# Kernel tuning notes

Measured on AMD Instinct MI355X. Metric: run time of the kernel, lower is better.

Reference implementation:

```python
import jax, jax.numpy as jnp
import numpy as np

ROUTES = 1152
CAPS = 10
IN_CH = 8
OUT_CH = 16
BATCH = 256
NUM_ITER = 3


def setup_inputs() -> dict:
    key = jax.random.key(0)
    kx, kw = jax.random.split(key)
    x = jax.random.normal(kx, (BATCH, ROUTES, IN_CH), dtype=jnp.float32)
    # W corresponds to nn.Parameter of shape [1, routes, caps, out, in]; leading 1 dropped.
    W = jax.random.normal(kw, (ROUTES, CAPS, OUT_CH, IN_CH), dtype=jnp.float32)
    return {"x": x, "W": W}


def _squash(s):
    # Faithful to source: sum of squares over the trailing singleton dim -> elementwise.
    sq = s * s
    return sq * s / ((1.0 + sq) * jnp.sqrt(sq))


def reference(x, W):
    # u_hat[b,r,c,o] = W[r,c,o,i] @ x[b,r,i]
    u_hat = jnp.einsum("rcoi,bri->brco", W, x)
    b_ij = jnp.zeros((ROUTES, CAPS), dtype=x.dtype)
    v = None
    for it in range(NUM_ITER):
        # legacy F.softmax on 4D [1,R,C,1] tensor -> softmax over dim=1 (routes)
        c_ij = jax.nn.softmax(b_ij, axis=0)  # [R, C]
        s_j = jnp.einsum("rc,brco->bco", c_ij, u_hat)  # [B, C, O]
        v = _squash(s_j)
        if it < NUM_ITER - 1:
            # a_ij[b,r,c] = <u_hat[b,r,c,:], v[b,c,:]>; b_ij += mean over batch
            a_ij = jnp.einsum("brco,bco->brc", u_hat, v)
            b_ij = b_ij + a_ij.mean(axis=0)
    # original returns v_j.squeeze(1) with shape [B, caps, out, 1]
    return v[..., None]
```

## Files before the change

### kernel.cpp

```cpp
#include <hip/hip_runtime.h>
#include <math.h>

namespace {

constexpr int B_ = 256;
constexpr int R_ = 1152;
constexpr int C_ = 10;
constexpr int O_ = 16;
constexpr int I_ = 8;
constexpr int CO_ = C_ * O_;
constexpr int WRI_ = C_ * O_ * I_;

constexpr int KS_  = 64;
constexpr int RC_  = R_ / KS_;

constexpr int NRP_ = 576;
constexpr int NBA_ = NRP_ * 2;

constexpr int KSF_ = 16;
constexpr int RCF_ = R_ / KSF_;
constexpr int MBF_ = 16;

constexpr size_t XT_OFF    = 0;
constexpr size_t XT_N      = (size_t)R_ * B_ * I_;
constexpr size_t SA_OFF    = XT_OFF + XT_N;
constexpr size_t SAB_N     = (size_t)CO_ * B_;
constexpr size_t SB_OFF    = SA_OFF + SAB_N;
constexpr size_t BIJ_OFF   = SB_OFF + SAB_N;
constexpr size_t BIJ_N     = (size_t)C_ * R_;
constexpr size_t ZERO_N    = 2 * SAB_N + BIJ_N;
constexpr size_t FL_TOTAL  = BIJ_OFF + BIJ_N;

__device__ __forceinline__ float rcp_fast(float x) {
#if defined(__has_builtin)
#if __has_builtin(__builtin_amdgcn_rcpf)
    return __builtin_amdgcn_rcpf(x);
#else
    return 1.0f / x;
#endif
#else
    return 1.0f / x;
#endif
}

__device__ __forceinline__ float squashf(float s) {
    return s * fabsf(s) / (1.0f + s * s);
}

__device__ __forceinline__ float squash_fast(float s) {
    return s * fabsf(s) * rcp_fast(1.0f + s * s);
}

__global__ __launch_bounds__(256) void k_tr(const float* __restrict__ x,
                                            float* __restrict__ xT,
                                            float* __restrict__ zbase) {
    __shared__ float t[8][32][8];
    const int tid = threadIdx.x;
    {
        const int gi = blockIdx.x * 256 + tid;
        if (gi < (int)(ZERO_N / 4))
            ((float4*)zbase)[gi] = make_float4(0.f, 0.f, 0.f, 0.f);
    }
    const int r0 = (blockIdx.x % 36) * 32;
    const int b0 = (blockIdx.x / 36) * 8;
    {
        const int rl = tid & 31, bl = tid >> 5;
        const float4* p = (const float4*)(x + ((size_t)(b0 + bl) * R_ + (r0 + rl)) * I_);
        const float4 a0 = p[0], a1 = p[1];
        float* d = &t[bl][rl][0];
        *(float4*)d = a0;
        *(float4*)(d + 4) = a1;
    }
    __syncthreads();
    {
        const int f = tid & 7, rw = tid >> 3;
        const float* s8 = &t[f][rw][0];
        const float4 a0 = *(const float4*)s8, a1 = *(const float4*)(s8 + 4);
        float* d = xT + ((size_t)(r0 + rw) * B_ + (b0 + f)) * I_;
        *(float4*)d = a0;
        *(float4*)(d + 4) = a1;
    }
}

template <bool UNIFORM>
__global__ __launch_bounds__(256) void k_s8(const float* __restrict__ xT,
                                            const float* __restrict__ Wm,
                                            const float* __restrict__ bijT,
                                            float* __restrict__ s_dst) {
    __shared__ __align__(16) float wl[RC_ * 128];
    __shared__ float cwch[RC_];
    __shared__ float sred[8];

    const int tid   = threadIdx.x;
    const int lane  = tid & 63;
    const int bid   = blockIdx.x;
    const int c     = bid >> 7;
    const int chunk = bid & 127;
    const int ks    = chunk >> 1;
    const int bh    = chunk & 1;
    const int r0    = ks * RC_;

    if (!UNIFORM) {
        const float* bc = bijT + (size_t)c * R_;
        float bv[5];
        float m = -1e30f;
        #pragma unroll
        for (int k = 0; k < 5; ++k) {
            const int r = tid + 256 * k;
            bv[k] = (r < R_) ? bc[r] : -1e30f;
            m = fmaxf(m, bv[k]);
        }
        #pragma unroll
        for (int off = 32; off > 0; off >>= 1)
            m = fmaxf(m, __shfl_down(m, off, 64));
        if (lane == 0) sred[tid >> 6] = m;
        __syncthreads();
        const float bm = fmaxf(fmaxf(sred[0], sred[1]), fmaxf(sred[2], sred[3]));
        float se = 0.f;
        #pragma unroll
        for (int k = 0; k < 5; ++k)
            se += (bv[k] > -1e29f) ? expf(bv[k] - bm) : 0.f;
        #pragma unroll
        for (int off = 32; off > 0; off >>= 1)
            se += __shfl_down(se, off, 64);
        if (lane == 0) sred[4 + (tid >> 6)] = se;
        __syncthreads();
        const float inv = 1.0f / (sred[4] + sred[5] + sred[6] + sred[7]);
        if (tid < RC_) cwch[tid] = expf(bc[r0 + tid] - bm) * inv;
        __syncthreads();
    }

    {
        const float4* src = (const float4*)(Wm + ((size_t)r0 * C_ + c) * 128);
        float4* dst = (float4*)wl;
        #pragma unroll
        for (int k = 0; k < (RC_ * 32 + 255) / 256; ++k) {
            const int idx = tid + 256 * k;
            if (idx < RC_ * 32) {
                const int r = idx >> 5, q = idx & 31;
                float4 wv = src[(size_t)r * (C_ * 32) + q];
                const float cw = UNIFORM ? (1.0f / (float)R_) : cwch[r];
                wv.x *= cw; wv.y *= cw; wv.z *= cw; wv.w *= cw;
                dst[idx] = wv;
            }
        }
    }
    __syncthreads();

    const int o0 = (tid >> 6) * 4;
    const float* xbase = xT + ((size_t)r0 * B_ + bh * 128 + lane) * I_;

    float acc[4][2];
    #pragma unroll
    for (int oo = 0; oo < 4; ++oo) { acc[oo][0] = 0.f; acc[oo][1] = 0.f; }

    #pragma unroll 2
    for (int r = 0; r < RC_; ++r) {
        const float* xr = xbase + (size_t)r * B_ * I_;
        const float4 a00 = ((const float4*)xr)[0];
        const float4 a01 = ((const float4*)xr)[1];
        const float4 a10 = ((const float4*)(xr + 64 * I_))[0];
        const float4 a11 = ((const float4*)(xr + 64 * I_))[1];
        const float4* wp = (const float4*)&wl[r * 128 + o0 * 8];
        #pragma unroll
        for (int oo = 0; oo < 4; ++oo) {
            const float4 w0 = wp[oo * 2 + 0];
            const float4 w1 = wp[oo * 2 + 1];
            float a = acc[oo][0];
            a = fmaf(a00.x, w0.x, a);
            a = fmaf(a00.y, w0.y, a);
            a = fmaf(a00.z, w0.z, a);
            a = fmaf(a00.w, w0.w, a);
            a = fmaf(a01.x, w1.x, a);
            a = fmaf(a01.y, w1.y, a);
            a = fmaf(a01.z, w1.z, a);
            a = fmaf(a01.w, w1.w, a);
            acc[oo][0] = a;
            float b = acc[oo][1];
            b = fmaf(a10.x, w0.x, b);
            b = fmaf(a10.y, w0.y, b);
            b = fmaf(a10.z, w0.z, b);
            b = fmaf(a10.w, w0.w, b);
            b = fmaf(a11.x, w1.x, b);
            b = fmaf(a11.y, w1.y, b);
            b = fmaf(a11.z, w1.z, b);
            b = fmaf(a11.w, w1.w, b);
            acc[oo][1] = b;
        }
    }

    float* sp = s_dst + (size_t)(c * O_ + o0) * B_ + bh * 128 + lane;
    #pragma unroll
    for (int oo = 0; oo < 4; ++oo) {
        atomicAdd(sp + (size_t)oo * B_, acc[oo][0]);
        atomicAdd(sp + (size_t)oo * B_ + 64, acc[oo][1]);
    }
}

struct A9Sh {
    float4 xsw[2 * 256];
    float  part[2][320];
};

__global__ __launch_bounds__(320) void k_a9(const float* __restrict__ xT,
                                            const float* __restrict__ Wm,
                                            const float* __restrict__ s_read,
                                            float* __restrict__ s_zero,
                                            float* __restrict__ bijT) {
    __shared__ A9Sh sh;
    const int tid = threadIdx.x;
    const int bid = blockIdx.x;
    const int bh  = (bid >= NRP_) ? 1 : 0;
    const int rp  = bid - bh * NRP_;
    const int r0  = rp * 2;

    if (s_zero != nullptr && bid < 40 && tid < 256) {
        ((float4*)s_zero)[bid * 256 + tid] = make_float4(0.f, 0.f, 0.f, 0.f);
    }

    {
        const float4* src = (const float4*)(xT + (size_t)r0 * B_ * I_);
        for (int k = tid; k < 2 * 256; k += 320) {
            const int rr = k >> 8, rem = k & 255;
            sh.xsw[k ^ ((k >> 5) & 7)] = src[rr * 512 + bh * 256 + rem];
        }
    }
    __syncthreads();

    const int cq = tid % 40;
    const int bg = tid / 40;
    const int b0 = bg * 16;

    float acc[2][4][8];
    #pragma unroll
    for (int rr = 0; rr < 2; ++rr)
        #pragma unroll
        for (int j = 0; j < 4; ++j)
            #pragma unroll
            for (int i = 0; i < 8; ++i) acc[rr][j][i] = 0.f;

    const float* vbase = s_read + (size_t)(4 * cq) * B_ + bh * 128 + b0;

    #pragma unroll 2
    for (int bb = 0; bb < 16; bb += 4) {
        float va[4][4];
        #pragma unroll
        for (int j = 0; j < 4; ++j) {
            const float4 t = *(const float4*)(vbase + (size_t)j * B_ + bb);
            va[j][0] = squash_fast(t.x);
            va[j][1] = squash_fast(t.y);
            va[j][2] = squash_fast(t.z);
            va[j][3] = squash_fast(t.w);
        }
        #pragma unroll
        for (int j2 = 0; j2 < 4; ++j2) {
            const int eb = (b0 + bb + j2) * 2;
            #pragma unroll
            for (int rr = 0; rr < 2; ++rr) {
                const float4 x0 = sh.xsw[(rr * 256 + eb) ^ bg];
                const float4 x1 = sh.xsw[(rr * 256 + eb + 1) ^ bg];
                #pragma unroll
                for (int j = 0; j < 4; ++j) {
                    const float w = va[j][j2];
                    acc[rr][j][0] = fmaf(w, x0.x, acc[rr][j][0]);
                    acc[rr][j][1] = fmaf(w, x0.y, acc[rr][j][1]);
                    acc[rr][j][2] = fmaf(w, x0.z, acc[rr][j][2]);
                    acc[rr][j][3] = fmaf(w, x0.w, acc[rr][j][3]);
                    acc[rr][j][4] = fmaf(w, x1.x, acc[rr][j][4]);
                    acc[rr][j][5] = fmaf(w, x1.y, acc[rr][j][5]);
                    acc[rr][j][6] = fmaf(w, x1.z, acc[rr][j][6]);
                    acc[rr][j][7] = fmaf(w, x1.w, acc[rr][j][7]);
                }
            }
        }
    }

    #pragma unroll
    for (int rr = 0; rr < 2; ++rr) {
        const float* wp = Wm + (((size_t)(r0 + rr)) * CO_ + 4 * cq) * I_;
        float psum = 0.f;
        #pragma unroll
        for (int j = 0; j < 4; ++j) {
            const float4 w0 = *(const float4*)(wp + j * 8);
            const float4 w1 = *(const float4*)(wp + j * 8 + 4);
            float p = acc[rr][j][0] * w0.x;
            p = fmaf(acc[rr][j][1], w0.y, p);
            p = fmaf(acc[rr][j][2], w0.z, p);
            p = fmaf(acc[rr][j][3], w0.w, p);
            p = fmaf(acc[rr][j][4], w1.x, p);
            p = fmaf(acc[rr][j][5], w1.y, p);
            p = fmaf(acc[rr][j][6], w1.z, p);
            p = fmaf(acc[rr][j][7], w1.w, p);
            psum += p;
        }
        sh.part[rr][tid] = psum;
    }
    __syncthreads();

    if (tid < 2 * C_) {
        const int r = tid / C_, c2 = tid % C_;
        float s = 0.f;
        #pragma unroll
        for (int g2 = 0; g2 < 8; ++g2)
            #pragma unroll
            for (int q = 0; q < 4; ++q)
                s += sh.part[r][g2 * 40 + c2 * 4 + q];
        atomicAdd(&bijT[(size_t)c2 * R_ + (r0 + r)], s * (1.0f / (float)B_));
    }
}

__global__ __launch_bounds__(256) void k_sqout(const float* __restrict__ s,
                                               float* __restrict__ out) {
    const int co = blockIdx.x;
    const int b  = threadIdx.x;
    out[(size_t)b * CO_ + co] = squash_fast(s[(size_t)co * B_ + b]);
}

template <bool UNIFORM>
__global__ __launch_bounds__(256) void k_s_f(const float* __restrict__ x,
                                             const float* __restrict__ Wm,
                                             const float* __restrict__ cij,
                                             float* __restrict__ s_out) {
    const int o  = threadIdx.x & 15;
    const int tb = threadIdx.x >> 4;
    const int b  = blockIdx.z * MBF_ + tb;
    const int c  = blockIdx.y;
    const int r0 = blockIdx.x * RCF_;

    const float* xp = x + ((size_t)b * R_ + r0) * I_;
    const float* wp = Wm + (((size_t)r0 * C_ + c) * O_ + o) * I_;
    const float* cp = cij + (size_t)r0 * C_ + c;

    float acc = 0.f;
    #pragma unroll 4
    for (int r = 0; r < RCF_; ++r) {
        const float4 xv0 = *(const float4*)(xp);
        const float4 xv1 = *(const float4*)(xp + 4);
        const float4 wv0 = *(const float4*)(wp);
        const float4 wv1 = *(const float4*)(wp + 4);
        const float p0 = fmaf(xv0.y, wv0.y, xv0.x * wv0.x);
        const float p1 = fmaf(xv0.w, wv0.w, xv0.z * wv0.z);
        const float p2 = fmaf(xv1.y, wv1.y, xv1.x * wv1.x);
        const float p3 = fmaf(xv1.w, wv1.w, xv1.z * wv1.z);
        const float cw = UNIFORM ? (1.0f / (float)R_) : cp[0];
        acc = fmaf(cw, (p0 + p1) + (p2 + p3), acc);
        xp += I_;
        wp += WRI_;
        cp += C_;
    }
    atomicAdd(&s_out[((size_t)b * C_ + c) * O_ + o], acc);
}

__global__ __launch_bounds__(256) void k_a_f(const float* __restrict__ x,
                                             const float* __restrict__ Wm,
                                             const float* __restrict__ s_in,
                                             float* __restrict__ amean) {
    __shared__ __align__(16) float wlds[2 * WRI_];
    __shared__ float red[4][2 * C_];

    const int tid = threadIdx.x;
    const int r0  = blockIdx.x * 2;

    const float* wsrc = Wm + (size_t)r0 * WRI_;
    #pragma unroll
    for (int k = 0; k < 2 * WRI_ / 256; ++k)
        wlds[tid + 256 * k] = wsrc[tid + 256 * k];
    __syncthreads();

    const int b    = tid;
    const int lane = tid & 63;
    const int wv   = tid >> 6;

    float xv[2][I_];
    const float4* xp4 = (const float4*)(x + ((size_t)b * R_ + r0) * I_);
    #pragma unroll
    for (int rr = 0; rr < 2; ++rr) {
        const float4 a0 = xp4[rr * 2 + 0];
        const float4 a1 = xp4[rr * 2 + 1];
        xv[rr][0] = a0.x; xv[rr][1] = a0.y; xv[rr][2] = a0.z; xv[rr][3] = a0.w;
        xv[rr][4] = a1.x; xv[rr][5] = a1.y; xv[rr][6] = a1.z; xv[rr][7] = a1.w;
    }

    #pragma unroll 1
    for (int c = 0; c < C_; ++c) {
        const float4* sp4 = (const float4*)(s_in + ((size_t)b * C_ + c) * O_);
        float v[O_];
        #pragma unroll
        for (int q = 0; q < 4; ++q) {
            const float4 sv = sp4[q];
            v[q * 4 + 0] = squashf(sv.x);
            v[q * 4 + 1] = squashf(sv.y);
            v[q * 4 + 2] = squashf(sv.z);
            v[q * 4 + 3] = squashf(sv.w);
        }
        #pragma unroll 1
        for (int rr = 0; rr < 2; ++rr) {
            const float4* wl4 = (const float4*)&wlds[(rr * C_ + c) * O_ * I_];
            float a = 0.f;
            #pragma unroll
            for (int o = 0; o < O_; ++o) {
                const float4 w0 = wl4[o * 2 + 0];
                const float4 w1 = wl4[o * 2 + 1];
                float u = xv[rr][0] * w0.x;
                u = fmaf(xv[rr][1], w0.y, u);
                u = fmaf(xv[rr][2], w0.z, u);
                u = fmaf(xv[rr][3], w0.w, u);
                u = fmaf(xv[rr][4], w1.x, u);
                u = fmaf(xv[rr][5], w1.y, u);
                u = fmaf(xv[rr][6], w1.z, u);
                u = fmaf(xv[rr][7], w1.w, u);
                a = fmaf(u, v[o], a);
            }
            #pragma unroll
            for (int off = 32; off > 0; off >>= 1)
                a += __shfl_down(a, off, 64);
            if (lane == 0) red[wv][rr * C_ + c] = a;
        }
    }

    __syncthreads();
    if (tid < 2 * C_) {
        const float t = red[0][tid] + red[1][tid] + red[2][tid] + red[3][tid];
        const int rr = tid / C_;
        const int c  = tid % C_;
        amean[(size_t)(r0 + rr) * C_ + c] = t * (1.0f / (float)B_);
    }
}

__global__ __launch_bounds__(256) void k_soft(const float* __restrict__ amean,
                                              float* __restrict__ bij,
                                              float* __restrict__ cij) {
    const int c   = blockIdx.x;
    const int tid = threadIdx.x;
    __shared__ float sred[4];

    float vals[5];
    float m = -1e30f;
    #pragma unroll
    for (int k = 0; k < 5; ++k) {
        const int r = tid + 256 * k;
        if (r < R_) {
            const size_t idx = (size_t)r * C_ + c;
            const float vv = bij[idx] + amean[idx];
            bij[idx] = vv;
            vals[k] = vv;
            m = fmaxf(m, vv);
        } else {
            vals[k] = -1e30f;
        }
    }
    #pragma unroll
    for (int off = 32; off > 0; off >>= 1)
        m = fmaxf(m, __shfl_down(m, off, 64));
    if ((tid & 63) == 0) sred[tid >> 6] = m;
    __syncthreads();
    const float bm = fmaxf(fmaxf(sred[0], sred[1]), fmaxf(sred[2], sred[3]));
    __syncthreads();

    float se = 0.f;
    #pragma unroll
    for (int k = 0; k < 5; ++k)
        se += (vals[k] > -1e29f) ? expf(vals[k] - bm) : 0.f;
    #pragma unroll
    for (int off = 32; off > 0; off >>= 1)
        se += __shfl_down(se, off, 64);
    if ((tid & 63) == 0) sred[tid >> 6] = se;
    __syncthreads();
    const float inv = 1.0f / (sred[0] + sred[1] + sred[2] + sred[3]);

    #pragma unroll
    for (int k = 0; k < 5; ++k) {
        const int r = tid + 256 * k;
        if (r < R_) cij[(size_t)r * C_ + c] = expf(vals[k] - bm) * inv;
    }
}

__global__ __launch_bounds__(256) void k_squash(float* __restrict__ s) {
    const int idx = blockIdx.x * 256 + threadIdx.x;
    if (idx < B_ * CO_) s[idx] = squashf(s[idx]);
}

}

extern "C" void kernel_launch(void* const* d_in, const int* in_sizes, int n_in,
                              void* d_out, int out_size, void* d_ws, size_t ws_size,
                              hipStream_t stream) {
    const float* x  = (const float*)d_in[0];
    const float* Wm = (const float*)d_in[1];
    float* out = (float*)d_out;
    float* ws  = (float*)d_ws;

    const size_t need = FL_TOTAL * sizeof(float);

    if (ws_size >= need) {
        float* xT   = ws + XT_OFF;
        float* sA   = ws + SA_OFF;
        float* sB   = ws + SB_OFF;
        float* bijT = ws + BIJ_OFF;

        k_tr<<<1152, 256, 0, stream>>>(x, xT, sA );

        k_s8<true><<<C_ * 128, 256, 0, stream>>>(xT, Wm, bijT, sA);
        k_a9<<<NBA_, 320, 0, stream>>>(xT, Wm, sA, nullptr, bijT);

        k_s8<false><<<C_ * 128, 256, 0, stream>>>(xT, Wm, bijT, sB);
        k_a9<<<NBA_, 320, 0, stream>>>(xT, Wm, sB, sA , bijT);

        k_s8<false><<<C_ * 128, 256, 0, stream>>>(xT, Wm, bijT, sA);
        k_sqout<<<CO_, 256, 0, stream>>>(sA, out);
    } else {
        float* s_buf = ws;
        float* cij   = ws + 40960;
        float* bij   = cij + R_ * C_;
        float* amean = bij + R_ * C_;

        const dim3 gsf(KSF_, C_, B_ / MBF_);

        hipMemsetAsync(bij, 0, R_ * C_ * sizeof(float), stream);

        hipMemsetAsync(s_buf, 0, B_ * CO_ * sizeof(float), stream);
        k_s_f<true><<<gsf, 256, 0, stream>>>(x, Wm, cij, s_buf);
        k_a_f<<<R_ / 2, 256, 0, stream>>>(x, Wm, s_buf, amean);
        k_soft<<<C_, 256, 0, stream>>>(amean, bij, cij);

        hipMemsetAsync(s_buf, 0, B_ * CO_ * sizeof(float), stream);
        k_s_f<false><<<gsf, 256, 0, stream>>>(x, Wm, cij, s_buf);
        k_a_f<<<R_ / 2, 256, 0, stream>>>(x, Wm, s_buf, amean);
        k_soft<<<C_, 256, 0, stream>>>(amean, bij, cij);

        hipMemsetAsync(out, 0, B_ * CO_ * sizeof(float), stream);
        k_s_f<false><<<gsf, 256, 0, stream>>>(x, Wm, cij, out);
        k_squash<<<(B_ * CO_ + 255) / 256, 256, 0, stream>>>(out);
    }
}
```

Measured before the change: 202.0 us.

## Precompute squashed v transposed and restructure s/a kernels per route

The s-kernel now gives each block all 256 batches (4 per thread) instead of splitting the batch in halves, so each W tile is loaded and scaled once and the grid is halved. A new small transpose kernel squashes s once into a batch-major vT buffer, so the agreement kernel no longer recomputes squash per element. The agreement kernel now handles one route over the full batch per block and writes b_ij with a plain add instead of atomics. The cost is an extra launch per iteration, more registers in the s-kernel, and fewer blocks, which may reduce occupancy.

```diff
diff --git a/kernel.cpp b/kernel.cpp
--- a/kernel.cpp
+++ b/kernel.cpp
@@ -13,9 +13,6 @@
 
 constexpr int KS_  = 64;
 constexpr int RC_  = R_ / KS_;
-
-constexpr int NRP_ = 576;
-constexpr int NBA_ = NRP_ * 2;
 
 constexpr int KSF_ = 16;
 constexpr int RCF_ = R_ / KSF_;
@@ -29,7 +26,9 @@
 constexpr size_t BIJ_OFF   = SB_OFF + SAB_N;
 constexpr size_t BIJ_N     = (size_t)C_ * R_;
 constexpr size_t ZERO_N    = 2 * SAB_N + BIJ_N;
-constexpr size_t FL_TOTAL  = BIJ_OFF + BIJ_N;
+constexpr size_t VT_OFF    = BIJ_OFF + BIJ_N;
+constexpr size_t VT_N      = (size_t)B_ * CO_;
+constexpr size_t FL_TOTAL  = VT_OFF + VT_N;
 
 __device__ __forceinline__ float rcp_fast(float x) {
 #if defined(__has_builtin)
@@ -83,7 +82,7 @@
 }
 
 template <bool UNIFORM>
-__global__ __launch_bounds__(256) void k_s8(const float* __restrict__ xT,
+__global__ __launch_bounds__(256) void k_s9(const float* __restrict__ xT,
                                             const float* __restrict__ Wm,
                                             const float* __restrict__ bijT,
                                             float* __restrict__ s_dst) {
@@ -91,14 +90,12 @@
     __shared__ float cwch[RC_];
     __shared__ float sred[8];
 
-    const int tid   = threadIdx.x;
-    const int lane  = tid & 63;
-    const int bid   = blockIdx.x;
-    const int c     = bid >> 7;
-    const int chunk = bid & 127;
-    const int ks    = chunk >> 1;
-    const int bh    = chunk & 1;
-    const int r0    = ks * RC_;
+    const int tid  = threadIdx.x;
+    const int lane = tid & 63;
+    const int bid  = blockIdx.x;
+    const int c    = bid >> 6;
+    const int ks   = bid & 63;
+    const int r0   = ks * RC_;
 
     if (!UNIFORM) {
         const float* bc = bijT + (size_t)c * R_;
@@ -148,164 +145,177 @@
     __syncthreads();
 
     const int o0 = (tid >> 6) * 4;
-    const float* xbase = xT + ((size_t)r0 * B_ + bh * 128 + lane) * I_;
-
-    float acc[4][2];
-    #pragma unroll
-    for (int oo = 0; oo < 4; ++oo) { acc[oo][0] = 0.f; acc[oo][1] = 0.f; }
+    const float* xbase = xT + ((size_t)r0 * B_ + lane) * I_;
+
+    float acc[4][4];
+    #pragma unroll
+    for (int oo = 0; oo < 4; ++oo)
+        #pragma unroll
+        for (int bb = 0; bb < 4; ++bb) acc[oo][bb] = 0.f;
 
     #pragma unroll 2
     for (int r = 0; r < RC_; ++r) {
         const float* xr = xbase + (size_t)r * B_ * I_;
-        const float4 a00 = ((const float4*)xr)[0];
-        const float4 a01 = ((const float4*)xr)[1];
-        const float4 a10 = ((const float4*)(xr + 64 * I_))[0];
-        const float4 a11 = ((const float4*)(xr + 64 * I_))[1];
+        float4 xa[4][2];
+        #pragma unroll
+        for (int bb = 0; bb < 4; ++bb) {
+            const float4* xp = (const float4*)(xr + (size_t)bb * 64 * I_);
+            xa[bb][0] = xp[0];
+            xa[bb][1] = xp[1];
+        }
         const float4* wp = (const float4*)&wl[r * 128 + o0 * 8];
         #pragma unroll
         for (int oo = 0; oo < 4; ++oo) {
             const float4 w0 = wp[oo * 2 + 0];
             const float4 w1 = wp[oo * 2 + 1];
-            float a = acc[oo][0];
-            a = fmaf(a00.x, w0.x, a);
-            a = fmaf(a00.y, w0.y, a);
-            a = fmaf(a00.z, w0.z, a);
-            a = fmaf(a00.w, w0.w, a);
-            a = fmaf(a01.x, w1.x, a);
-            a = fmaf(a01.y, w1.y, a);
-            a = fmaf(a01.z, w1.z, a);
-            a = fmaf(a01.w, w1.w, a);
-            acc[oo][0] = a;
-            float b = acc[oo][1];
-            b = fmaf(a10.x, w0.x, b);
-            b = fmaf(a10.y, w0.y, b);
-            b = fmaf(a10.z, w0.z, b);
-            b = fmaf(a10.w, w0.w, b);
-            b = fmaf(a11.x, w1.x, b);
-            b = fmaf(a11.y, w1.y, b);
-            b = fmaf(a11.z, w1.z, b);
-            b = fmaf(a11.w, w1.w, b);
-            acc[oo][1] = b;
-        }
-    }
-
-    float* sp = s_dst + (size_t)(c * O_ + o0) * B_ + bh * 128 + lane;
-    #pragma unroll
-    for (int oo = 0; oo < 4; ++oo) {
-        atomicAdd(sp + (size_t)oo * B_, acc[oo][0]);
-        atomicAdd(sp + (size_t)oo * B_ + 64, acc[oo][1]);
-    }
-}
-
-struct A9Sh {
-    float4 xsw[2 * 256];
-    float  part[2][320];
+            #pragma unroll
+            for (int bb = 0; bb < 4; ++bb) {
+                float a = acc[oo][bb];
+                a = fmaf(xa[bb][0].x, w0.x, a);
+                a = fmaf(xa[bb][0].y, w0.y, a);
+                a = fmaf(xa[bb][0].z, w0.z, a);
+                a = fmaf(xa[bb][0].w, w0.w, a);
+                a = fmaf(xa[bb][1].x, w1.x, a);
+                a = fmaf(xa[bb][1].y, w1.y, a);
+                a = fmaf(xa[bb][1].z, w1.z, a);
+                a = fmaf(xa[bb][1].w, w1.w, a);
+                acc[oo][bb] = a;
+            }
+        }
+    }
+
+    float* sp = s_dst + (size_t)(c * O_ + o0) * B_ + lane;
+    #pragma unroll
+    for (int oo = 0; oo < 4; ++oo)
+        #pragma unroll
+        for (int bb = 0; bb < 4; ++bb)
+            atomicAdd(sp + (size_t)oo * B_ + bb * 64, acc[oo][bb]);
+}
+
+__global__ __launch_bounds__(256) void k_vt(const float* __restrict__ s,
+                                            float* __restrict__ vT) {
+    __shared__ float t[32][65];
+    const int tid  = threadIdx.x;
+    const int co0  = (blockIdx.x % 5) * 32;
+    const int b0   = (blockIdx.x / 5) * 64;
+    const int lane = tid & 63;
+    const int g    = tid >> 6;
+    #pragma unroll
+    for (int k = 0; k < 8; ++k) {
+        const int co = g + k * 4;
+        t[co][lane] = s[(size_t)(co0 + co) * B_ + b0 + lane];
+    }
+    __syncthreads();
+    const int bl  = tid >> 2;
+    const int coq = (tid & 3) * 8;
+    float* dst = vT + (size_t)(b0 + bl) * CO_ + co0 + coq;
+    float4 o0, o1;
+    o0.x = squash_fast(t[coq + 0][bl]);
+    o0.y = squash_fast(t[coq + 1][bl]);
+    o0.z = squash_fast(t[coq + 2][bl]);
+    o0.w = squash_fast(t[coq + 3][bl]);
+    o1.x = squash_fast(t[coq + 4][bl]);
+    o1.y = squash_fast(t[coq + 5][bl]);
+    o1.z = squash_fast(t[coq + 6][bl]);
+    o1.w = squash_fast(t[coq + 7][bl]);
+    *(float4*)dst = o0;
+    *(float4*)(dst + 4) = o1;
+}
+
+struct A10Sh {
+    float4 xsw[512];
+    float  part[320];
 };
 
-__global__ __launch_bounds__(320) void k_a9(const float* __restrict__ xT,
-                                            const float* __restrict__ Wm,
-                                            const float* __restrict__ s_read,
-                                            float* __restrict__ s_zero,
-                                            float* __restrict__ bijT) {
-    __shared__ A9Sh sh;
+__global__ __launch_bounds__(320) void k_a10(const float* __restrict__ xT,
+                                             const float* __restrict__ Wm,
+                                             const float* __restrict__ vT,
+                                             float* __restrict__ s_zero,
+                                             float* __restrict__ bijT) {
+    __shared__ A10Sh sh;
     const int tid = threadIdx.x;
-    const int bid = blockIdx.x;
-    const int bh  = (bid >= NRP_) ? 1 : 0;
-    const int rp  = bid - bh * NRP_;
-    const int r0  = rp * 2;
-
-    if (s_zero != nullptr && bid < 40 && tid < 256) {
-        ((float4*)s_zero)[bid * 256 + tid] = make_float4(0.f, 0.f, 0.f, 0.f);
+    const int r   = blockIdx.x;
+
+    if (s_zero != nullptr && r < 40 && tid < 256) {
+        ((float4*)s_zero)[r * 256 + tid] = make_float4(0.f, 0.f, 0.f, 0.f);
     }
 
     {
-        const float4* src = (const float4*)(xT + (size_t)r0 * B_ * I_);
-        for (int k = tid; k < 2 * 256; k += 320) {
-            const int rr = k >> 8, rem = k & 255;
-            sh.xsw[k ^ ((k >> 5) & 7)] = src[rr * 512 + bh * 256 + rem];
-        }
+        const float4* src = (const float4*)(xT + (size_t)r * B_ * I_);
+        for (int k = tid; k < 512; k += 320)
+            sh.xsw[k ^ ((k >> 6) & 7)] = src[k];
     }
     __syncthreads();
 
     const int cq = tid % 40;
     const int bg = tid / 40;
-    const int b0 = bg * 16;
-
-    float acc[2][4][8];
-    #pragma unroll
-    for (int rr = 0; rr < 2; ++rr)
-        #pragma unroll
-        for (int j = 0; j < 4; ++j)
+    const int b0 = bg * 32;
+
+    float acc[4][8];
+    #pragma unroll
+    for (int j = 0; j < 4; ++j)
+        #pragma unroll
+        for (int i = 0; i < 8; ++i) acc[j][i] = 0.f;
+
+    const float* vb = vT + (size_t)b0 * CO_ + 4 * cq;
+
+    #pragma unroll 2
+    for (int bb = 0; bb < 32; bb += 4) {
+        float va[4][4];
+        #pragma unroll
+        for (int j2 = 0; j2 < 4; ++j2) {
+            const float4 t = *(const float4*)(vb + (size_t)(bb + j2) * CO_);
+            va[j2][0] = t.x; va[j2][1] = t.y; va[j2][2] = t.z; va[j2][3] = t.w;
+        }
+        #pragma unroll
+        for (int j2 = 0; j2 < 4; ++j2) {
+            const int e0 = ((b0 + bb + j2) * 2) ^ bg;
+            const float4 x0 = sh.xsw[e0];
+            const float4 x1 = sh.xsw[e0 ^ 1];
             #pragma unroll
-            for (int i = 0; i < 8; ++i) acc[rr][j][i] = 0.f;
-
-    const float* vbase = s_read + (size_t)(4 * cq) * B_ + bh * 128 + b0;
-
-    #pragma unroll 2
-    for (int bb = 0; bb < 16; bb += 4) {
-        float va[4][4];
-        #pragma unroll
-        for (int j = 0; j < 4; ++j) {
-            const float4 t = *(const float4*)(vbase + (size_t)j * B_ + bb);
-            va[j][0] = squash_fast(t.x);
-            va[j][1] = squash_fast(t.y);
-            va[j][2] = squash_fast(t.z);
-            va[j][3] = squash_fast(t.w);
-        }
-        #pragma unroll
-        for (int j2 = 0; j2 < 4; ++j2) {
-            const int eb = (b0 + bb + j2) * 2;
-            #pragma unroll
-            for (int rr = 0; rr < 2; ++rr) {
-                const float4 x0 = sh.xsw[(rr * 256 + eb) ^ bg];
-                const float4 x1 = sh.xsw[(rr * 256 + eb + 1) ^ bg];
-                #pragma unroll
-                for (int j = 0; j < 4; ++j) {
-                    const float w = va[j][j2];
-                    acc[rr][j][0] = fmaf(w, x0.x, acc[rr][j][0]);
-                    acc[rr][j][1] = fmaf(w, x0.y, acc[rr][j][1]);
-                    acc[rr][j][2] = fmaf(w, x0.z, acc[rr][j][2]);
-                    acc[rr][j][3] = fmaf(w, x0.w, acc[rr][j][3]);
-                    acc[rr][j][4] = fmaf(w, x1.x, acc[rr][j][4]);
-                    acc[rr][j][5] = fmaf(w, x1.y, acc[rr][j][5]);
-                    acc[rr][j][6] = fmaf(w, x1.z, acc[rr][j][6]);
-                    acc[rr][j][7] = fmaf(w, x1.w, acc[rr][j][7]);
-                }
+            for (int j = 0; j < 4; ++j) {
+                const float w = va[j2][j];
+                acc[j][0] = fmaf(w, x0.x, acc[j][0]);
+                acc[j][1] = fmaf(w, x0.y, acc[j][1]);
+                acc[j][2] = fmaf(w, x0.z, acc[j][2]);
+                acc[j][3] = fmaf(w, x0.w, acc[j][3]);
+                acc[j][4] = fmaf(w, x1.x, acc[j][4]);
+                acc[j][5] = fmaf(w, x1.y, acc[j][5]);
+                acc[j][6] = fmaf(w, x1.z, acc[j][6]);
+                acc[j][7] = fmaf(w, x1.w, acc[j][7]);
             }
         }
     }
 
-    #pragma unroll
-    for (int rr = 0; rr < 2; ++rr) {
-        const float* wp = Wm + (((size_t)(r0 + rr)) * CO_ + 4 * cq) * I_;
+    {
+        const float* wp = Wm + ((size_t)r * CO_ + 4 * cq) * I_;
         float psum = 0.f;
         #pragma unroll
         for (int j = 0; j < 4; ++j) {
             const float4 w0 = *(const float4*)(wp + j * 8);
             const float4 w1 = *(const float4*)(wp + j * 8 + 4);
-            float p = acc[rr][j][0] * w0.x;
-            p = fmaf(acc[rr][j][1], w0.y, p);
-            p = fmaf(acc[rr][j][2], w0.z, p);
-            p = fmaf(acc[rr][j][3], w0.w, p);
-            p = fmaf(acc[rr][j][4], w1.x, p);
-            p = fmaf(acc[rr][j][5], w1.y, p);
-            p = fmaf(acc[rr][j][6], w1.z, p);
-            p = fmaf(acc[rr][j][7], w1.w, p);
+            float p = acc[j][0] * w0.x;
+            p = fmaf(acc[j][1], w0.y, p);
+            p = fmaf(acc[j][2], w0.z, p);
+            p = fmaf(acc[j][3], w0.w, p);
+            p = fmaf(acc[j][4], w1.x, p);
+            p = fmaf(acc[j][5], w1.y, p);
+            p = fmaf(acc[j][6], w1.z, p);
+            p = fmaf(acc[j][7], w1.w, p);
             psum += p;
         }
-        sh.part[rr][tid] = psum;
-    }
-    __syncthreads();
-
-    if (tid < 2 * C_) {
-        const int r = tid / C_, c2 = tid % C_;
+        sh.part[tid] = psum;
+    }
+    __syncthreads();
+
+    if (tid < C_) {
         float s = 0.f;
         #pragma unroll
         for (int g2 = 0; g2 < 8; ++g2)
             #pragma unroll
             for (int q = 0; q < 4; ++q)
-                s += sh.part[r][g2 * 40 + c2 * 4 + q];
-        atomicAdd(&bijT[(size_t)c2 * R_ + (r0 + r)], s * (1.0f / (float)B_));
+                s += sh.part[g2 * 40 + tid * 4 + q];
+        bijT[(size_t)tid * R_ + r] += s * (1.0f / (float)B_);
     }
 }
 
@@ -497,16 +507,19 @@
         float* sA   = ws + SA_OFF;
         float* sB   = ws + SB_OFF;
         float* bijT = ws + BIJ_OFF;
+        float* vTb  = ws + VT_OFF;
 
         k_tr<<<1152, 256, 0, stream>>>(x, xT, sA );
 
-        k_s8<true><<<C_ * 128, 256, 0, stream>>>(xT, Wm, bijT, sA);
-        k_a9<<<NBA_, 320, 0, stream>>>(xT, Wm, sA, nullptr, bijT);
-
-        k_s8<false><<<C_ * 128, 256, 0, stream>>>(xT, Wm, bijT, sB);
-        k_a9<<<NBA_, 320, 0, stream>>>(xT, Wm, sB, sA , bijT);
-
-        k_s8<false><<<C_ * 128, 256, 0, stream>>>(xT, Wm, bijT, sA);
+        k_s9<true><<<C_ * KS_, 256, 0, stream>>>(xT, Wm, bijT, sA);
+        k_vt<<<20, 256, 0, stream>>>(sA, vTb);
+        k_a10<<<R_, 320, 0, stream>>>(xT, Wm, vTb, nullptr, bijT);
+
+        k_s9<false><<<C_ * KS_, 256, 0, stream>>>(xT, Wm, bijT, sB);
+        k_vt<<<20, 256, 0, stream>>>(sB, vTb);
+        k_a10<<<R_, 320, 0, stream>>>(xT, Wm, vTb, sA , bijT);
+
+        k_s9<false><<<C_ * KS_, 256, 0, stream>>>(xT, Wm, bijT, sA);
         k_sqout<<<CO_, 256, 0, stream>>>(sA, out);
     } else {
         float* s_buf = ws;
```

Result: faster. 177.1 us (-12.3%).
